# Performance work log

Hardware: AMD Instinct MI355X
Metric: run time of the kernel (lower is better)

## Reference

```python
import jax, jax.numpy as jnp
import numpy as np

DIM_MODEL = 1024
NUM_HEADS = 16
HEAD_DIM = DIM_MODEL // NUM_HEADS
NEG = -1000000000.0


def setup_inputs() -> dict:
    key = jax.random.key(0)
    ks = jax.random.split(key, 11)
    B, S, D = 2, 2048, DIM_MODEL
    s = 1.0 / np.sqrt(D)
    return {
        "q": jax.random.normal(ks[0], (B, S, D), jnp.float32),
        "k": jax.random.normal(ks[1], (B, S, D), jnp.float32),
        "v": jax.random.normal(ks[2], (B, S, D), jnp.float32),
        "Wq": jax.random.normal(ks[3], (D, D), jnp.float32) * s,
        "bq": jnp.zeros((D,), jnp.float32),
        "Wk": jax.random.normal(ks[4], (D, D), jnp.float32) * s,
        "bk": jnp.zeros((D,), jnp.float32),
        "Wv": jax.random.normal(ks[5], (D, D), jnp.float32) * s,
        "bv": jnp.zeros((D,), jnp.float32),
        "Wo": jax.random.normal(ks[6], (D, D), jnp.float32) * s,
        "bo": jnp.zeros((D,), jnp.float32),
    }


def reference(q, k, v, Wq, bq, Wk, bk, Wv, bv, Wo, bo):
    B, S, D = q.shape
    H, hd = NUM_HEADS, HEAD_DIM

    def proj(x, W, b):
        # torch Linear: x @ W.T + b, then split heads -> [B, H, S, hd]
        y = jnp.einsum("bsd,ed->bse", x, W) + b
        return y.reshape(B, S, H, hd).transpose(0, 2, 1, 3)

    qh = proj(q, Wq, bq)
    kh = proj(k, Wk, bk)
    vh = proj(v, Wv, bv)

    scores = jnp.einsum("bhqd,bhkd->bhqk", qh, kh) / np.sqrt(hd)
    # torch.triu(ones(S,S), diagonal=0): upper triangle INCLUDING diagonal is masked
    mask = jnp.triu(jnp.ones((S, S), bool))
    scores = jnp.where(mask, NEG, scores)
    # softmax over dim=-2 (query axis), as in the original module
    attn = jax.nn.softmax(scores, axis=-2)
    ctx = jnp.einsum("bhqk,bhkd->bhqd", attn, vh)  # [B,H,S,hd]
    ctx = ctx.transpose(0, 2, 1, 3).reshape(B, S, D)
    return jnp.einsum("bsd,ed->bse", ctx, Wo) + bo
```

## Files before the change

kernel.cpp:

```cpp
#include <hip/hip_runtime.h>

typedef __bf16 bf16;
typedef __attribute__((ext_vector_type(8))) __bf16 bf16x8;
typedef __attribute__((ext_vector_type(2))) __bf16 bf16x2;
typedef __attribute__((ext_vector_type(4))) float f32x4;

#define AS1 __attribute__((address_space(1)))
#define AS3 __attribute__((address_space(3)))

#define BB 2
#define SS 2048
#define DD 1024
#define HH 16
#define HD 64
#define BH (BB*HH)

#define QSCALE 0.1803368801111244f

static __device__ __forceinline__ f32x4 mfma16(bf16x8 a, bf16x8 b, f32x4 c) {
  return __builtin_amdgcn_mfma_f32_16x16x32_bf16(a, b, c, 0, 0, 0);
}
static __device__ __forceinline__ float fexp2(float x) {
  return __builtin_amdgcn_exp2f(x);
}

static __device__ __forceinline__ void swz512(int bid, int& bh, int& pr) {
  int c = bid & 7, j = bid >> 3;
  bh = c + 8 * (j & 3);
  pr = j >> 2;
}
static __device__ __forceinline__ void swz1024(int bid, int& bh, int& strip0, int& qh) {
  int c = bid & 7, j = bid >> 3;
  bh = c + 8 * (j & 3);
  int rem = j >> 2;
  strip0 = rem & 15;
  qh = rem >> 4;
}

__global__ __launch_bounds__(256) void cvt_w(const float* __restrict__ s0, const float* __restrict__ s1,
                                             const float* __restrict__ s2, const float* __restrict__ s3,
                                             bf16* __restrict__ o0, bf16* __restrict__ o1,
                                             bf16* __restrict__ o2, bf16* __restrict__ o3) {
  const int z = blockIdx.y;
  const float* s = (z == 0) ? s0 : (z == 1) ? s1 : (z == 2) ? s2 : s3;
  bf16* o = (z == 0) ? o0 : (z == 1) ? o1 : (z == 2) ? o2 : o3;
  int i = blockIdx.x * 256 + threadIdx.x;
  const float4* sp = (const float4*)s;
  float4 a = sp[2 * i], b = sp[2 * i + 1];
  bf16x8 v;
  v[0] = (bf16)a.x; v[1] = (bf16)a.y; v[2] = (bf16)a.z; v[3] = (bf16)a.w;
  v[4] = (bf16)b.x; v[5] = (bf16)b.y; v[6] = (bf16)b.z; v[7] = (bf16)b.w;
  ((bf16x8*)o)[i] = v;
}

__global__ __launch_bounds__(256) void cvt_x(const float* __restrict__ s0, const float* __restrict__ s1,
                                             const float* __restrict__ s2,
                                             bf16* __restrict__ o0, bf16* __restrict__ o1,
                                             bf16* __restrict__ o2) {
  const int z = blockIdx.y;
  const float* s = (z == 0) ? s0 : (z == 1) ? s1 : s2;
  bf16* o = (z == 0) ? o0 : (z == 1) ? o1 : o2;
  int i = blockIdx.x * 256 + threadIdx.x;
  const float4* sp = (const float4*)s;
  float4 a = sp[2 * i], b = sp[2 * i + 1];
  bf16x8 v;
  v[0] = (bf16)a.x; v[1] = (bf16)a.y; v[2] = (bf16)a.z; v[3] = (bf16)a.w;
  v[4] = (bf16)b.x; v[5] = (bf16)b.y; v[6] = (bf16)b.z; v[7] = (bf16)b.w;
  ((bf16x8*)o)[i] = v;
}

__device__ __forceinline__ void gemm_core(const bf16* __restrict__ A,
                                          const bf16* __restrict__ Bm, int K,
                                          int m0, int n0, int w, int l,
                                          bf16* sA, bf16* sB, f32x4 (&acc)[4][4]) {
  const int l15 = l & 15, lg = l >> 4;
  const int wr = (w >> 1) * 64, wc = (w & 1) * 64;
  for (int kt = 0; kt < K; kt += 32) {
#pragma unroll
    for (int i = 0; i < 2; ++i) {
      int t = i * 256 + w * 64 + l;
      const bf16* ga = A + (size_t)(m0 + (t >> 2)) * K + kt + (t & 3) * 8;
      const bf16* gb = Bm + (size_t)(n0 + (t >> 2)) * K + kt + (t & 3) * 8;
      __builtin_amdgcn_global_load_lds((const AS1 void*)ga,
                                       (AS3 void*)(sA + (i * 256 + w * 64) * 8), 16, 0, 0);
      __builtin_amdgcn_global_load_lds((const AS1 void*)gb,
                                       (AS3 void*)(sB + (i * 256 + w * 64) * 8), 16, 0, 0);
    }
    __syncthreads();
    bf16x8 af[4], bfr[4];
#pragma unroll
    for (int m = 0; m < 4; ++m)
      af[m] = *(const bf16x8*)(sA + (wr + m * 16 + l15) * 32 + lg * 8);
#pragma unroll
    for (int n = 0; n < 4; ++n)
      bfr[n] = *(const bf16x8*)(sB + (wc + n * 16 + l15) * 32 + lg * 8);
#pragma unroll
    for (int m = 0; m < 4; ++m)
#pragma unroll
      for (int n = 0; n < 4; ++n)
        acc[m][n] = mfma16(af[m], bfr[n], acc[m][n]);
    __syncthreads();
  }
}

__global__ __launch_bounds__(256) void proj_gemm(
    const bf16* __restrict__ Xq, const bf16* __restrict__ Xk, const bf16* __restrict__ Xv,
    const bf16* __restrict__ Wq, const bf16* __restrict__ Wk, const bf16* __restrict__ Wv,
    const float* __restrict__ bq, const float* __restrict__ bk, const float* __restrict__ bv,
    bf16* __restrict__ Oq, bf16* __restrict__ Ok, bf16* __restrict__ Ovt) {
  __shared__ __align__(16) bf16 sA[128 * 32];
  __shared__ __align__(16) bf16 sB[128 * 32];
  const int z = blockIdx.z;
  const bf16* A = (z == 0) ? Xq : ((z == 1) ? Xk : Xv);
  const bf16* W = (z == 0) ? Wq : ((z == 1) ? Wk : Wv);
  const float* bias = (z == 0) ? bq : ((z == 1) ? bk : bv);
  const int tid = threadIdx.x, l = tid & 63, w = tid >> 6;
  const int m0 = blockIdx.y * 128, n0 = blockIdx.x * 128;
  f32x4 acc[4][4] = {};
  gemm_core(A, W, DD, m0, n0, w, l, sA, sB, acc);
  const int l15 = l & 15, lg = l >> 4;
  const int wr = (w >> 1) * 64, wc = (w & 1) * 64;
#pragma unroll
  for (int n = 0; n < 4; ++n) {
    int col = n0 + wc + n * 16 + l15;
    float bb = bias[col];
    int h = col >> 6, d = col & 63;
#pragma unroll
    for (int m = 0; m < 4; ++m) {
#pragma unroll
      for (int r = 0; r < 4; ++r) {
        int row = m0 + wr + m * 16 + lg * 4 + r;
        int b = row >> 11, s = row & (SS - 1);
        float vv = acc[m][n][r] + bb;
        if (z == 0) vv *= QSCALE;
        if (z != 2)
          ((z == 0) ? Oq : Ok)[(((size_t)(b * HH + h)) * SS + s) * HD + d] = (bf16)vv;
        else
          Ovt[(((size_t)(b * HH + h)) * HD + d) * SS + s] = (bf16)vv;
      }
    }
  }
}

__global__ __launch_bounds__(256) void out_gemm(const bf16* __restrict__ A,
                                                const bf16* __restrict__ W,
                                                const float* __restrict__ bias,
                                                float* __restrict__ out) {
  __shared__ __align__(16) bf16 sA[128 * 32];
  __shared__ __align__(16) bf16 sB[128 * 32];
  const int tid = threadIdx.x, l = tid & 63, w = tid >> 6;
  const int m0 = blockIdx.y * 128, n0 = blockIdx.x * 128;
  f32x4 acc[4][4] = {};
  gemm_core(A, W, DD, m0, n0, w, l, sA, sB, acc);
  const int l15 = l & 15, lg = l >> 4;
  const int wr = (w >> 1) * 64, wc = (w & 1) * 64;
#pragma unroll
  for (int n = 0; n < 4; ++n) {
    int col = n0 + wc + n * 16 + l15;
    float bb = bias[col];
#pragma unroll
    for (int m = 0; m < 4; ++m)
#pragma unroll
      for (int r = 0; r < 4; ++r) {
        int row = m0 + wr + m * 16 + lg * 4 + r;
        out[(size_t)row * DD + col] = acc[m][n][r] + bb;
      }
  }
}

__global__ __launch_bounds__(256) void colz(const bf16* __restrict__ Qb,
                                            const bf16* __restrict__ Kb,
                                            float* __restrict__ zPart) {
  __shared__ float zred[4][64];
  int bh, pair, qh;
  swz1024(blockIdx.x, bh, pair, qh);
  const int tid = threadIdx.x, l = tid & 63, w = tid >> 6;
  const int l15 = l & 15, lg = l >> 4;
  const bf16* Q = Qb + (size_t)bh * SS * HD;
  const bf16* Kh = Kb + (size_t)bh * SS * HD;

  for (int half = 0; half < 2; ++half) {
    const int s = half ? (31 - pair) : pair;
    const int c0 = s * 64;
    bf16x8 kf[4][2];
#pragma unroll
    for (int kt = 0; kt < 4; ++kt) {
      kf[kt][0] = *(const bf16x8*)&Kh[(c0 + kt * 16 + l15) * HD + lg * 8];
      kf[kt][1] = *(const bf16x8*)&Kh[(c0 + kt * 16 + l15) * HD + 32 + lg * 8];
    }
    float z[4] = {};
    const int qstart = c0 + qh * 64 + w * 16;
    bf16x8 qa0, qa1, qn0, qn1;
    if (qstart < SS) {
      qa0 = *(const bf16x8*)&Q[(qstart + l15) * HD + lg * 8];
      qa1 = *(const bf16x8*)&Q[(qstart + l15) * HD + 32 + lg * 8];
    }
    for (int qb = qstart; qb < SS; qb += 128) {
      const int qnext = qb + 128;
      if (qnext < SS) {
        qn0 = *(const bf16x8*)&Q[(qnext + l15) * HD + lg * 8];
        qn1 = *(const bf16x8*)&Q[(qnext + l15) * HD + 32 + lg * 8];
      }
      f32x4 d[4] = {};
#pragma unroll
      for (int kt = 0; kt < 4; ++kt) {
        d[kt] = mfma16(qa0, kf[kt][0], d[kt]);
        d[kt] = mfma16(qa1, kf[kt][1], d[kt]);
      }
#pragma unroll
      for (int kt = 0; kt < 4; ++kt) {
        const int kcol = c0 + kt * 16 + l15;
#pragma unroll
        for (int r = 0; r < 4; ++r) {
          int qq = qb + lg * 4 + r;
          z[kt] += (qq > kcol) ? fexp2(d[kt][r]) : 0.f;
        }
      }
      qa0 = qn0; qa1 = qn1;
    }
#pragma unroll
    for (int kt = 0; kt < 4; ++kt) {
      z[kt] += __shfl_xor(z[kt], 16);
      z[kt] += __shfl_xor(z[kt], 32);
    }
    if (l < 16) {
#pragma unroll
      for (int kt = 0; kt < 4; ++kt) zred[w][kt * 16 + l15] = z[kt];
    }
    __syncthreads();
    if (tid < 64) {
      float zs = zred[0][tid] + zred[1][tid] + zred[2][tid] + zred[3][tid];
      zPart[((size_t)qh * BH + bh) * SS + c0 + tid] = zs;
    }
    __syncthreads();
  }
}

__global__ __launch_bounds__(256, 2) void attn_ctx(const bf16* __restrict__ Qb,
                                                   const bf16* __restrict__ Kb,
                                                   const bf16* __restrict__ Vt,
                                                   const float* __restrict__ zPart,
                                                   bf16* __restrict__ ctx) {
  __shared__ __align__(16) float red[3][64 * 68];
  int bh, pr;
  swz512(blockIdx.x, bh, pr);
  const int tid = threadIdx.x, l = tid & 63, w = tid >> 6;
  const int l15 = l & 15, lg = l >> 4;
  const bf16* Q = Qb + (size_t)bh * SS * HD;
  const bf16* Kh = Kb + (size_t)bh * SS * HD;
  const bf16* V = Vt + (size_t)bh * HD * SS;
  const float* zp0 = zPart + (size_t)bh * SS;
  const float* zp1 = zPart + ((size_t)BH + bh) * SS;
  const int b = bh >> 4, h = bh & 15;

  float vlast[4];
#pragma unroll
  for (int dt = 0; dt < 4; ++dt)
    vlast[dt] = (float)V[(size_t)(dt * 16 + l15) * SS + (SS - 1)] * (1.0f / (float)SS);

  for (int half = 0; half < 2; ++half) {
    const int t = half ? (31 - pr) : pr;
    const int q0 = t * 64;

    bf16x8 qa[4][2];
#pragma unroll
    for (int qt = 0; qt < 4; ++qt)
#pragma unroll
      for (int kk = 0; kk < 2; ++kk)
        qa[qt][kk] = *(const bf16x8*)&Q[(q0 + qt * 16 + l15) * HD + kk * 32 + lg * 8];

    f32x4 acc[4][4] = {};
    const int kend = q0 + 64;
    for (int k0 = w * 32; k0 < kend; k0 += 128) {
      bf16x8 ka0 = *(const bf16x8*)&Kh[(k0 + l15) * HD + lg * 8];
      bf16x8 ka1 = *(const bf16x8*)&Kh[(k0 + l15) * HD + 32 + lg * 8];
      bf16x8 kb0 = *(const bf16x8*)&Kh[(k0 + 16 + l15) * HD + lg * 8];
      bf16x8 kb1 = *(const bf16x8*)&Kh[(k0 + 16 + l15) * HD + 32 + lg * 8];
      union { unsigned int u[4]; bf16x8 v; } vf[4];
#pragma unroll
      for (int dt = 0; dt < 4; ++dt) {
        const bf16* vrow = &V[(size_t)(dt * 16 + l15) * SS];
        uint2 lo = *(const uint2*)&vrow[k0 + 4 * lg];
        uint2 hi = *(const uint2*)&vrow[k0 + 16 + 4 * lg];
        vf[dt].u[0] = lo.x; vf[dt].u[1] = lo.y; vf[dt].u[2] = hi.x; vf[dt].u[3] = hi.y;
      }
      f32x4 za0 = *(const f32x4*)&zp0[k0 + lg * 4];
      f32x4 zb0 = *(const f32x4*)&zp1[k0 + lg * 4];
      f32x4 za1 = *(const f32x4*)&zp0[k0 + 16 + lg * 4];
      f32x4 zb1 = *(const f32x4*)&zp1[k0 + 16 + lg * 4];
      f32x4 rz0, rz1;
#pragma unroll
      for (int r = 0; r < 4; ++r) {
        float s0 = za0[r] + zb0[r], s1 = za1[r] + zb1[r];
        rz0[r] = (s0 > 0.f) ? 1.0f / s0 : 0.f;
        rz1[r] = (s1 > 0.f) ? 1.0f / s1 : 0.f;
      }
      f32x4 s[4][2];
#pragma unroll
      for (int qt = 0; qt < 4; ++qt) {
        f32x4 z0 = {}, z1 = {};
        z0 = mfma16(ka0, qa[qt][0], z0);
        z0 = mfma16(ka1, qa[qt][1], z0);
        z1 = mfma16(kb0, qa[qt][0], z1);
        z1 = mfma16(kb1, qa[qt][1], z1);
        s[qt][0] = z0; s[qt][1] = z1;
      }
      const int kb0i = k0 + lg * 4, kb1i = k0 + 16 + lg * 4;
#pragma unroll
      for (int qt = 0; qt < 4; ++qt) {
        const int qq = q0 + qt * 16 + l15;
        union { unsigned int u[4]; bf16x8 v; } pa;
#pragma unroll
        for (int hw = 0; hw < 2; ++hw) {
          bf16x2 t0, t1;
#pragma unroll
          for (int r = 0; r < 2; ++r) {
            int rr = hw * 2 + r;
            float p0 = fexp2(s[qt][0][rr]) * ((kb0i + rr < qq) ? rz0[rr] : 0.f);
            float p1 = fexp2(s[qt][1][rr]) * ((kb1i + rr < qq) ? rz1[rr] : 0.f);
            t0[r] = (bf16)p0;
            t1[r] = (bf16)p1;
          }
          pa.u[hw] = __builtin_bit_cast(unsigned int, t0);
          pa.u[hw + 2] = __builtin_bit_cast(unsigned int, t1);
        }
#pragma unroll
        for (int dt = 0; dt < 4; ++dt)
          acc[qt][dt] = mfma16(pa.v, vf[dt].v, acc[qt][dt]);
      }
    }

    if (w) {
      float* buf = red[w - 1];
#pragma unroll
      for (int qt = 0; qt < 4; ++qt)
#pragma unroll
        for (int dt = 0; dt < 4; ++dt)
          *(f32x4*)&buf[(dt * 16 + l15) * 68 + qt * 16 + lg * 4] = acc[qt][dt];
    }
    __syncthreads();
    if (w == 0) {
#pragma unroll
      for (int qt = 0; qt < 4; ++qt) {
#pragma unroll
        for (int dt = 0; dt < 4; ++dt) {
          f32x4 a = acc[qt][dt];
#pragma unroll
          for (int j = 0; j < 3; ++j)
            a += *(const f32x4*)&red[j][(dt * 16 + l15) * 68 + qt * 16 + lg * 4];
#pragma unroll
          for (int r = 0; r < 4; ++r) {
            int q = q0 + qt * 16 + lg * 4 + r;
            ctx[((size_t)(b * SS + q)) * DD + h * HD + dt * 16 + l15] =
                (bf16)(a[r] + vlast[dt]);
          }
        }
      }
    }
    __syncthreads();
  }
}

extern "C" void kernel_launch(void* const* d_in, const int* in_sizes, int n_in,
                              void* d_out, int out_size, void* d_ws, size_t ws_size,
                              hipStream_t stream) {
  const float* q  = (const float*)d_in[0];
  const float* k  = (const float*)d_in[1];
  const float* v  = (const float*)d_in[2];
  const float* Wq = (const float*)d_in[3];
  const float* bq = (const float*)d_in[4];
  const float* Wk = (const float*)d_in[5];
  const float* bk = (const float*)d_in[6];
  const float* Wv = (const float*)d_in[7];
  const float* bv = (const float*)d_in[8];
  const float* Wo = (const float*)d_in[9];
  const float* bo = (const float*)d_in[10];

  char* ws = (char*)d_ws;
  const size_t SZP = (size_t)4096 * 1024 * 2;
  const size_t SZW = (size_t)1024 * 1024 * 2;
  bf16* Qb   = (bf16*)(ws + 0 * SZP);
  bf16* Kb   = (bf16*)(ws + 1 * SZP);
  bf16* Vt   = (bf16*)(ws + 2 * SZP);
  bf16* ctxb = (bf16*)(ws + 3 * SZP);
  bf16* qb16 = (bf16*)(ws + 4 * SZP);
  bf16* kb16 = (bf16*)(ws + 5 * SZP);
  bf16* vb16 = (bf16*)(ws + 6 * SZP);
  bf16* Wqb  = (bf16*)(ws + 7 * SZP + 0 * SZW);
  bf16* Wkb  = (bf16*)(ws + 7 * SZP + 1 * SZW);
  bf16* Wvb  = (bf16*)(ws + 7 * SZP + 2 * SZW);
  bf16* Wob  = (bf16*)(ws + 7 * SZP + 3 * SZW);
  float* zPart = (float*)(ws + 7 * SZP + 4 * SZW);

  cvt_w<<<dim3(512, 4), 256, 0, stream>>>(Wq, Wk, Wv, Wo, Wqb, Wkb, Wvb, Wob);
  cvt_x<<<dim3(2048, 3), 256, 0, stream>>>(q, k, v, qb16, kb16, vb16);

  proj_gemm<<<dim3(1024 / 128, 4096 / 128, 3), 256, 0, stream>>>(
      qb16, kb16, vb16, Wqb, Wkb, Wvb, bq, bk, bv, Qb, Kb, Vt);

  colz<<<1024, 256, 0, stream>>>(Qb, Kb, zPart);
  attn_ctx<<<512, 256, 0, stream>>>(Qb, Kb, Vt, zPart, ctxb);

  out_gemm<<<dim3(1024 / 128, 4096 / 128), 256, 0, stream>>>(ctxb, Wob, bo, (float*)d_out);
}
```

Before: 170.3 us.

## Halve attention query tile, precompute column reciprocals, specialize diagonal chunk

The attention-context kernel now processes 32-query tiles instead of 64, launching 1024 blocks with a higher occupancy hint and a smaller LDS reduction buffer. A new small kernel finalizes the column-sum reciprocals once, so attention blocks no longer recompute them. The key loop is split so that only the diagonal chunk applies the causal mask, handled by one wave. Smaller tiles reload K/V more often per query and add an extra launch, in exchange for more parallelism and less masking and divide work in the inner loop.

```diff
diff --git a/kernel.cpp b/kernel.cpp
--- a/kernel.cpp
+++ b/kernel.cpp
@@ -24,17 +24,17 @@
   return __builtin_amdgcn_exp2f(x);
 }
 
-static __device__ __forceinline__ void swz512(int bid, int& bh, int& pr) {
-  int c = bid & 7, j = bid >> 3;
-  bh = c + 8 * (j & 3);
-  pr = j >> 2;
-}
 static __device__ __forceinline__ void swz1024(int bid, int& bh, int& strip0, int& qh) {
   int c = bid & 7, j = bid >> 3;
   bh = c + 8 * (j & 3);
   int rem = j >> 2;
   strip0 = rem & 15;
   qh = rem >> 4;
+}
+static __device__ __forceinline__ void swzA(int bid, int& bh, int& pr) {
+  int c = bid & 7, j = bid >> 3;
+  bh = c + 8 * (j & 3);
+  pr = j >> 2;
 }
 
 __global__ __launch_bounds__(256) void cvt_w(const float* __restrict__ s0, const float* __restrict__ s1,
@@ -236,21 +236,89 @@
   }
 }
 
-__global__ __launch_bounds__(256, 2) void attn_ctx(const bf16* __restrict__ Qb,
+__global__ __launch_bounds__(256) void rzfin(const float* __restrict__ zPart,
+                                             float* __restrict__ cRZ) {
+  int i = blockIdx.x * 256 + threadIdx.x;
+  f32x4 a = ((const f32x4*)zPart)[i];
+  f32x4 b = ((const f32x4*)(zPart + (size_t)BH * SS))[i];
+  f32x4 r;
+#pragma unroll
+  for (int j = 0; j < 4; ++j) {
+    float s = a[j] + b[j];
+    r[j] = (s > 0.f) ? 1.0f / s : 0.f;
+  }
+  ((f32x4*)cRZ)[i] = r;
+}
+
+template <bool DIAG>
+static __device__ __forceinline__ void attn_chunk(
+    const bf16* __restrict__ Kh, const bf16* __restrict__ V,
+    const float* __restrict__ rzp, int k0, int q0,
+    const bf16x8 (&qa)[2][2], f32x4 (&acc)[2][4], int l15, int lg) {
+  bf16x8 ka0 = *(const bf16x8*)&Kh[(k0 + l15) * HD + lg * 8];
+  bf16x8 ka1 = *(const bf16x8*)&Kh[(k0 + l15) * HD + 32 + lg * 8];
+  bf16x8 kb0 = *(const bf16x8*)&Kh[(k0 + 16 + l15) * HD + lg * 8];
+  bf16x8 kb1 = *(const bf16x8*)&Kh[(k0 + 16 + l15) * HD + 32 + lg * 8];
+  union U { unsigned int u[4]; bf16x8 v; };
+  U vf[4];
+#pragma unroll
+  for (int dt = 0; dt < 4; ++dt) {
+    const bf16* vrow = &V[(size_t)(dt * 16 + l15) * SS];
+    uint2 lo = *(const uint2*)&vrow[k0 + 4 * lg];
+    uint2 hi = *(const uint2*)&vrow[k0 + 16 + 4 * lg];
+    vf[dt].u[0] = lo.x; vf[dt].u[1] = lo.y; vf[dt].u[2] = hi.x; vf[dt].u[3] = hi.y;
+  }
+  f32x4 rz0 = *(const f32x4*)&rzp[k0 + lg * 4];
+  f32x4 rz1 = *(const f32x4*)&rzp[k0 + 16 + lg * 4];
+  f32x4 s[2][2];
+#pragma unroll
+  for (int qt = 0; qt < 2; ++qt) {
+    f32x4 z0 = {}, z1 = {};
+    z0 = mfma16(ka0, qa[qt][0], z0);
+    z0 = mfma16(ka1, qa[qt][1], z0);
+    z1 = mfma16(kb0, qa[qt][0], z1);
+    z1 = mfma16(kb1, qa[qt][1], z1);
+    s[qt][0] = z0; s[qt][1] = z1;
+  }
+  const int kb0i = k0 + lg * 4, kb1i = k0 + 16 + lg * 4;
+#pragma unroll
+  for (int qt = 0; qt < 2; ++qt) {
+    const int qq = q0 + qt * 16 + l15;
+    U pa;
+#pragma unroll
+    for (int hw = 0; hw < 2; ++hw) {
+      bf16x2 t0, t1;
+#pragma unroll
+      for (int r = 0; r < 2; ++r) {
+        int rr = hw * 2 + r;
+        float m0 = DIAG ? ((kb0i + rr < qq) ? rz0[rr] : 0.f) : rz0[rr];
+        float m1 = DIAG ? ((kb1i + rr < qq) ? rz1[rr] : 0.f) : rz1[rr];
+        t0[r] = (bf16)(fexp2(s[qt][0][rr]) * m0);
+        t1[r] = (bf16)(fexp2(s[qt][1][rr]) * m1);
+      }
+      pa.u[hw] = __builtin_bit_cast(unsigned int, t0);
+      pa.u[hw + 2] = __builtin_bit_cast(unsigned int, t1);
+    }
+#pragma unroll
+    for (int dt = 0; dt < 4; ++dt)
+      acc[qt][dt] = mfma16(pa.v, vf[dt].v, acc[qt][dt]);
+  }
+}
+
+__global__ __launch_bounds__(256, 4) void attn_ctx(const bf16* __restrict__ Qb,
                                                    const bf16* __restrict__ Kb,
                                                    const bf16* __restrict__ Vt,
-                                                   const float* __restrict__ zPart,
+                                                   const float* __restrict__ cRZ,
                                                    bf16* __restrict__ ctx) {
-  __shared__ __align__(16) float red[3][64 * 68];
+  __shared__ __align__(16) float red[3][64 * 36];
   int bh, pr;
-  swz512(blockIdx.x, bh, pr);
+  swzA(blockIdx.x, bh, pr);
   const int tid = threadIdx.x, l = tid & 63, w = tid >> 6;
   const int l15 = l & 15, lg = l >> 4;
   const bf16* Q = Qb + (size_t)bh * SS * HD;
   const bf16* Kh = Kb + (size_t)bh * SS * HD;
   const bf16* V = Vt + (size_t)bh * HD * SS;
-  const float* zp0 = zPart + (size_t)bh * SS;
-  const float* zp1 = zPart + ((size_t)BH + bh) * SS;
+  const float* rzp = cRZ + (size_t)bh * SS;
   const int b = bh >> 4, h = bh & 15;
 
   float vlast[4];
@@ -259,95 +327,40 @@
     vlast[dt] = (float)V[(size_t)(dt * 16 + l15) * SS + (SS - 1)] * (1.0f / (float)SS);
 
   for (int half = 0; half < 2; ++half) {
-    const int t = half ? (31 - pr) : pr;
-    const int q0 = t * 64;
-
-    bf16x8 qa[4][2];
-#pragma unroll
-    for (int qt = 0; qt < 4; ++qt)
+    const int t = half ? (63 - pr) : pr;
+    const int q0 = t * 32;
+
+    bf16x8 qa[2][2];
+#pragma unroll
+    for (int qt = 0; qt < 2; ++qt)
 #pragma unroll
       for (int kk = 0; kk < 2; ++kk)
         qa[qt][kk] = *(const bf16x8*)&Q[(q0 + qt * 16 + l15) * HD + kk * 32 + lg * 8];
 
-    f32x4 acc[4][4] = {};
-    const int kend = q0 + 64;
-    for (int k0 = w * 32; k0 < kend; k0 += 128) {
-      bf16x8 ka0 = *(const bf16x8*)&Kh[(k0 + l15) * HD + lg * 8];
-      bf16x8 ka1 = *(const bf16x8*)&Kh[(k0 + l15) * HD + 32 + lg * 8];
-      bf16x8 kb0 = *(const bf16x8*)&Kh[(k0 + 16 + l15) * HD + lg * 8];
-      bf16x8 kb1 = *(const bf16x8*)&Kh[(k0 + 16 + l15) * HD + 32 + lg * 8];
-      union { unsigned int u[4]; bf16x8 v; } vf[4];
-#pragma unroll
-      for (int dt = 0; dt < 4; ++dt) {
-        const bf16* vrow = &V[(size_t)(dt * 16 + l15) * SS];
-        uint2 lo = *(const uint2*)&vrow[k0 + 4 * lg];
-        uint2 hi = *(const uint2*)&vrow[k0 + 16 + 4 * lg];
-        vf[dt].u[0] = lo.x; vf[dt].u[1] = lo.y; vf[dt].u[2] = hi.x; vf[dt].u[3] = hi.y;
-      }
-      f32x4 za0 = *(const f32x4*)&zp0[k0 + lg * 4];
-      f32x4 zb0 = *(const f32x4*)&zp1[k0 + lg * 4];
-      f32x4 za1 = *(const f32x4*)&zp0[k0 + 16 + lg * 4];
-      f32x4 zb1 = *(const f32x4*)&zp1[k0 + 16 + lg * 4];
-      f32x4 rz0, rz1;
-#pragma unroll
-      for (int r = 0; r < 4; ++r) {
-        float s0 = za0[r] + zb0[r], s1 = za1[r] + zb1[r];
-        rz0[r] = (s0 > 0.f) ? 1.0f / s0 : 0.f;
-        rz1[r] = (s1 > 0.f) ? 1.0f / s1 : 0.f;
-      }
-      f32x4 s[4][2];
-#pragma unroll
-      for (int qt = 0; qt < 4; ++qt) {
-        f32x4 z0 = {}, z1 = {};
-        z0 = mfma16(ka0, qa[qt][0], z0);
-        z0 = mfma16(ka1, qa[qt][1], z0);
-        z1 = mfma16(kb0, qa[qt][0], z1);
-        z1 = mfma16(kb1, qa[qt][1], z1);
-        s[qt][0] = z0; s[qt][1] = z1;
-      }
-      const int kb0i = k0 + lg * 4, kb1i = k0 + 16 + lg * 4;
-#pragma unroll
-      for (int qt = 0; qt < 4; ++qt) {
-        const int qq = q0 + qt * 16 + l15;
-        union { unsigned int u[4]; bf16x8 v; } pa;
-#pragma unroll
-        for (int hw = 0; hw < 2; ++hw) {
-          bf16x2 t0, t1;
-#pragma unroll
-          for (int r = 0; r < 2; ++r) {
-            int rr = hw * 2 + r;
-            float p0 = fexp2(s[qt][0][rr]) * ((kb0i + rr < qq) ? rz0[rr] : 0.f);
-            float p1 = fexp2(s[qt][1][rr]) * ((kb1i + rr < qq) ? rz1[rr] : 0.f);
-            t0[r] = (bf16)p0;
-            t1[r] = (bf16)p1;
-          }
-          pa.u[hw] = __builtin_bit_cast(unsigned int, t0);
-          pa.u[hw + 2] = __builtin_bit_cast(unsigned int, t1);
-        }
-#pragma unroll
-        for (int dt = 0; dt < 4; ++dt)
-          acc[qt][dt] = mfma16(pa.v, vf[dt].v, acc[qt][dt]);
-      }
-    }
+    f32x4 acc[2][4] = {};
+    for (int k0 = w * 32; k0 < q0; k0 += 128)
+      attn_chunk<false>(Kh, V, rzp, k0, q0, qa, acc, l15, lg);
+    if (w == (t & 3))
+      attn_chunk<true>(Kh, V, rzp, q0, q0, qa, acc, l15, lg);
 
     if (w) {
       float* buf = red[w - 1];
 #pragma unroll
-      for (int qt = 0; qt < 4; ++qt)
+      for (int qt = 0; qt < 2; ++qt)
 #pragma unroll
         for (int dt = 0; dt < 4; ++dt)
-          *(f32x4*)&buf[(dt * 16 + l15) * 68 + qt * 16 + lg * 4] = acc[qt][dt];
+          *(f32x4*)&buf[(dt * 16 + l15) * 36 + qt * 16 + lg * 4] = acc[qt][dt];
     }
     __syncthreads();
     if (w == 0) {
 #pragma unroll
-      for (int qt = 0; qt < 4; ++qt) {
+      for (int qt = 0; qt < 2; ++qt) {
 #pragma unroll
         for (int dt = 0; dt < 4; ++dt) {
           f32x4 a = acc[qt][dt];
 #pragma unroll
           for (int j = 0; j < 3; ++j)
-            a += *(const f32x4*)&red[j][(dt * 16 + l15) * 68 + qt * 16 + lg * 4];
+            a += *(const f32x4*)&red[j][(dt * 16 + l15) * 36 + qt * 16 + lg * 4];
 #pragma unroll
           for (int r = 0; r < 4; ++r) {
             int q = q0 + qt * 16 + lg * 4 + r;
@@ -391,6 +404,7 @@
   bf16* Wvb  = (bf16*)(ws + 7 * SZP + 2 * SZW);
   bf16* Wob  = (bf16*)(ws + 7 * SZP + 3 * SZW);
   float* zPart = (float*)(ws + 7 * SZP + 4 * SZW);
+  float* cRZ   = zPart + (size_t)2 * BH * SS;
 
   cvt_w<<<dim3(512, 4), 256, 0, stream>>>(Wq, Wk, Wv, Wo, Wqb, Wkb, Wvb, Wob);
   cvt_x<<<dim3(2048, 3), 256, 0, stream>>>(q, k, v, qb16, kb16, vb16);
@@ -399,7 +413,8 @@
       qb16, kb16, vb16, Wqb, Wkb, Wvb, bq, bk, bv, Qb, Kb, Vt);
 
   colz<<<1024, 256, 0, stream>>>(Qb, Kb, zPart);
-  attn_ctx<<<512, 256, 0, stream>>>(Qb, Kb, Vt, zPart, ctxb);
+  rzfin<<<(BH * SS / 4) / 256, 256, 0, stream>>>(zPart, cRZ);
+  attn_ctx<<<1024, 256, 0, stream>>>(Qb, Kb, Vt, cRZ, ctxb);
 
   out_gemm<<<dim3(1024 / 128, 4096 / 128), 256, 0, stream>>>(ctxb, Wob, bo, (float*)d_out);
 }
```

Result: slower. 214.5 us (+26.0%).

## Fold column-softmax reciprocal into V and double-buffer K/V loads in attn_ctx

Applied to the files above, without the earlier changes.

Adds two small kernels. One finalizes the per-key reciprocal column sums, and the other scales the transposed V in place by those reciprocals while also capturing the last-row V values. This removes the zPart loads, reciprocal math and per-element multiply from the attention inner loop. The inner loop now uses software-pipelined A/B register buffers for the K/V loads, and the causal mask is applied only to the diagonal 64-key tile, which is split between two waves. The cost is two extra launches, an extra pass over V, more register pressure, and the diagonal work now falling on only two of the four waves.

```diff
diff --git a/kernel.cpp b/kernel.cpp
--- a/kernel.cpp
+++ b/kernel.cpp
@@ -236,10 +236,107 @@
   }
 }
 
+__global__ __launch_bounds__(256) void rzfin(const float* __restrict__ zPart,
+                                             float* __restrict__ cRZ) {
+  int i = blockIdx.x * 256 + threadIdx.x;
+  f32x4 a = ((const f32x4*)zPart)[i];
+  f32x4 b = ((const f32x4*)(zPart + (size_t)BH * SS))[i];
+  f32x4 r;
+#pragma unroll
+  for (int j = 0; j < 4; ++j) {
+    float s = a[j] + b[j];
+    r[j] = (s > 0.f) ? 1.0f / s : 0.f;
+  }
+  ((f32x4*)cRZ)[i] = r;
+}
+
+__global__ __launch_bounds__(256) void vscale(bf16* __restrict__ Vt,
+                                              const float* __restrict__ cRZ,
+                                              float* __restrict__ vlastB) {
+  int i = blockIdx.x * 256 + threadIdx.x;
+  int sc = i & (SS / 8 - 1);
+  int rest = i >> 8;
+  int s0 = sc * 8;
+  bf16* p = Vt + (size_t)rest * SS + s0;
+  const float* rz = cRZ + (size_t)(rest >> 6) * SS + s0;
+  bf16x8 v = *(const bf16x8*)p;
+  if (s0 + 8 == SS) vlastB[rest] = (float)v[7] * (1.0f / (float)SS);
+  f32x4 r0 = *(const f32x4*)rz, r1 = *(const f32x4*)(rz + 4);
+  bf16x8 o;
+#pragma unroll
+  for (int j = 0; j < 4; ++j) o[j] = (bf16)((float)v[j] * r0[j]);
+#pragma unroll
+  for (int j = 0; j < 4; ++j) o[4 + j] = (bf16)((float)v[4 + j] * r1[j]);
+  *(bf16x8*)p = o;
+}
+
+struct KV {
+  bf16x8 k[4];
+  unsigned int v[4][4];
+};
+
+static __device__ __forceinline__ void kv_load(KV& b, const bf16* __restrict__ Kh,
+                                               const bf16* __restrict__ V, int k0,
+                                               int l15, int lg) {
+  b.k[0] = *(const bf16x8*)&Kh[(k0 + l15) * HD + lg * 8];
+  b.k[1] = *(const bf16x8*)&Kh[(k0 + l15) * HD + 32 + lg * 8];
+  b.k[2] = *(const bf16x8*)&Kh[(k0 + 16 + l15) * HD + lg * 8];
+  b.k[3] = *(const bf16x8*)&Kh[(k0 + 16 + l15) * HD + 32 + lg * 8];
+#pragma unroll
+  for (int dt = 0; dt < 4; ++dt) {
+    const bf16* vrow = &V[(size_t)(dt * 16 + l15) * SS];
+    uint2 lo = *(const uint2*)&vrow[k0 + 4 * lg];
+    uint2 hi = *(const uint2*)&vrow[k0 + 16 + 4 * lg];
+    b.v[dt][0] = lo.x; b.v[dt][1] = lo.y; b.v[dt][2] = hi.x; b.v[dt][3] = hi.y;
+  }
+}
+
+template <bool DIAG>
+static __device__ __forceinline__ void kv_compute(const KV& b, int k0, int q0,
+                                                  const bf16x8 (&qa)[4][2],
+                                                  f32x4 (&acc)[4][4], int l15, int lg) {
+  const int kb0i = k0 + lg * 4, kb1i = k0 + 16 + lg * 4;
+#pragma unroll
+  for (int qt = 0; qt < 4; ++qt) {
+    f32x4 s0 = {}, s1 = {};
+    s0 = mfma16(b.k[0], qa[qt][0], s0);
+    s0 = mfma16(b.k[1], qa[qt][1], s0);
+    s1 = mfma16(b.k[2], qa[qt][0], s1);
+    s1 = mfma16(b.k[3], qa[qt][1], s1);
+    const int qq = q0 + qt * 16 + l15;
+    union { unsigned int u[4]; bf16x8 v; } pa;
+#pragma unroll
+    for (int hw = 0; hw < 2; ++hw) {
+      bf16x2 t0, t1;
+#pragma unroll
+      for (int r = 0; r < 2; ++r) {
+        int rr = hw * 2 + r;
+        float p0 = fexp2(s0[rr]);
+        float p1 = fexp2(s1[rr]);
+        if (DIAG) {
+          p0 = (kb0i + rr < qq) ? p0 : 0.f;
+          p1 = (kb1i + rr < qq) ? p1 : 0.f;
+        }
+        t0[r] = (bf16)p0;
+        t1[r] = (bf16)p1;
+      }
+      pa.u[hw] = __builtin_bit_cast(unsigned int, t0);
+      pa.u[hw + 2] = __builtin_bit_cast(unsigned int, t1);
+    }
+#pragma unroll
+    for (int dt = 0; dt < 4; ++dt) {
+      union { unsigned int u[4]; bf16x8 v; } vf;
+      vf.u[0] = b.v[dt][0]; vf.u[1] = b.v[dt][1];
+      vf.u[2] = b.v[dt][2]; vf.u[3] = b.v[dt][3];
+      acc[qt][dt] = mfma16(pa.v, vf.v, acc[qt][dt]);
+    }
+  }
+}
+
 __global__ __launch_bounds__(256, 2) void attn_ctx(const bf16* __restrict__ Qb,
                                                    const bf16* __restrict__ Kb,
                                                    const bf16* __restrict__ Vt,
-                                                   const float* __restrict__ zPart,
+                                                   const float* __restrict__ vlastB,
                                                    bf16* __restrict__ ctx) {
   __shared__ __align__(16) float red[3][64 * 68];
   int bh, pr;
@@ -249,14 +346,11 @@
   const bf16* Q = Qb + (size_t)bh * SS * HD;
   const bf16* Kh = Kb + (size_t)bh * SS * HD;
   const bf16* V = Vt + (size_t)bh * HD * SS;
-  const float* zp0 = zPart + (size_t)bh * SS;
-  const float* zp1 = zPart + ((size_t)BH + bh) * SS;
   const int b = bh >> 4, h = bh & 15;
 
   float vlast[4];
 #pragma unroll
-  for (int dt = 0; dt < 4; ++dt)
-    vlast[dt] = (float)V[(size_t)(dt * 16 + l15) * SS + (SS - 1)] * (1.0f / (float)SS);
+  for (int dt = 0; dt < 4; ++dt) vlast[dt] = vlastB[bh * 64 + dt * 16 + l15];
 
   for (int half = 0; half < 2; ++half) {
     const int t = half ? (31 - pr) : pr;
@@ -270,63 +364,28 @@
         qa[qt][kk] = *(const bf16x8*)&Q[(q0 + qt * 16 + l15) * HD + kk * 32 + lg * 8];
 
     f32x4 acc[4][4] = {};
-    const int kend = q0 + 64;
-    for (int k0 = w * 32; k0 < kend; k0 += 128) {
-      bf16x8 ka0 = *(const bf16x8*)&Kh[(k0 + l15) * HD + lg * 8];
-      bf16x8 ka1 = *(const bf16x8*)&Kh[(k0 + l15) * HD + 32 + lg * 8];
-      bf16x8 kb0 = *(const bf16x8*)&Kh[(k0 + 16 + l15) * HD + lg * 8];
-      bf16x8 kb1 = *(const bf16x8*)&Kh[(k0 + 16 + l15) * HD + 32 + lg * 8];
-      union { unsigned int u[4]; bf16x8 v; } vf[4];
-#pragma unroll
-      for (int dt = 0; dt < 4; ++dt) {
-        const bf16* vrow = &V[(size_t)(dt * 16 + l15) * SS];
-        uint2 lo = *(const uint2*)&vrow[k0 + 4 * lg];
-        uint2 hi = *(const uint2*)&vrow[k0 + 16 + 4 * lg];
-        vf[dt].u[0] = lo.x; vf[dt].u[1] = lo.y; vf[dt].u[2] = hi.x; vf[dt].u[3] = hi.y;
-      }
-      f32x4 za0 = *(const f32x4*)&zp0[k0 + lg * 4];
-      f32x4 zb0 = *(const f32x4*)&zp1[k0 + lg * 4];
-      f32x4 za1 = *(const f32x4*)&zp0[k0 + 16 + lg * 4];
-      f32x4 zb1 = *(const f32x4*)&zp1[k0 + 16 + lg * 4];
-      f32x4 rz0, rz1;
-#pragma unroll
-      for (int r = 0; r < 4; ++r) {
-        float s0 = za0[r] + zb0[r], s1 = za1[r] + zb1[r];
-        rz0[r] = (s0 > 0.f) ? 1.0f / s0 : 0.f;
-        rz1[r] = (s1 > 0.f) ? 1.0f / s1 : 0.f;
-      }
-      f32x4 s[4][2];
-#pragma unroll
-      for (int qt = 0; qt < 4; ++qt) {
-        f32x4 z0 = {}, z1 = {};
-        z0 = mfma16(ka0, qa[qt][0], z0);
-        z0 = mfma16(ka1, qa[qt][1], z0);
-        z1 = mfma16(kb0, qa[qt][0], z1);
-        z1 = mfma16(kb1, qa[qt][1], z1);
-        s[qt][0] = z0; s[qt][1] = z1;
-      }
-      const int kb0i = k0 + lg * 4, kb1i = k0 + 16 + lg * 4;
-#pragma unroll
-      for (int qt = 0; qt < 4; ++qt) {
-        const int qq = q0 + qt * 16 + l15;
-        union { unsigned int u[4]; bf16x8 v; } pa;
-#pragma unroll
-        for (int hw = 0; hw < 2; ++hw) {
-          bf16x2 t0, t1;
-#pragma unroll
-          for (int r = 0; r < 2; ++r) {
-            int rr = hw * 2 + r;
-            float p0 = fexp2(s[qt][0][rr]) * ((kb0i + rr < qq) ? rz0[rr] : 0.f);
-            float p1 = fexp2(s[qt][1][rr]) * ((kb1i + rr < qq) ? rz1[rr] : 0.f);
-            t0[r] = (bf16)p0;
-            t1[r] = (bf16)p1;
-          }
-          pa.u[hw] = __builtin_bit_cast(unsigned int, t0);
-          pa.u[hw + 2] = __builtin_bit_cast(unsigned int, t1);
-        }
-#pragma unroll
-        for (int dt = 0; dt < 4; ++dt)
-          acc[qt][dt] = mfma16(pa.v, vf[dt].v, acc[qt][dt]);
+    KV A, B;
+    int k0 = w * 32;
+    if (k0 < q0) {
+      kv_load(A, Kh, V, k0, l15, lg);
+      for (;;) {
+        int kn = k0 + 128;
+        if (kn >= q0) { kv_compute<false>(A, k0, q0, qa, acc, l15, lg); break; }
+        kv_load(B, Kh, V, kn, l15, lg);
+        kv_compute<false>(A, k0, q0, qa, acc, l15, lg);
+        k0 = kn; kn += 128;
+        if (kn >= q0) { kv_compute<false>(B, k0, q0, qa, acc, l15, lg); break; }
+        kv_load(A, Kh, V, kn, l15, lg);
+        kv_compute<false>(B, k0, q0, qa, acc, l15, lg);
+        k0 = kn;
+      }
+    }
+    {
+      const int cw = (2 * t) & 3;
+      int dk = (w == cw) ? q0 : ((w == ((cw + 1) & 3)) ? q0 + 32 : -1);
+      if (dk >= 0) {
+        kv_load(A, Kh, V, dk, l15, lg);
+        kv_compute<true>(A, dk, q0, qa, acc, l15, lg);
       }
     }
 
@@ -391,6 +450,8 @@
   bf16* Wvb  = (bf16*)(ws + 7 * SZP + 2 * SZW);
   bf16* Wob  = (bf16*)(ws + 7 * SZP + 3 * SZW);
   float* zPart = (float*)(ws + 7 * SZP + 4 * SZW);
+  float* cRZ   = zPart + (size_t)2 * BH * SS;
+  float* vlastB = cRZ + (size_t)BH * SS;
 
   cvt_w<<<dim3(512, 4), 256, 0, stream>>>(Wq, Wk, Wv, Wo, Wqb, Wkb, Wvb, Wob);
   cvt_x<<<dim3(2048, 3), 256, 0, stream>>>(q, k, v, qb16, kb16, vb16);
@@ -399,7 +460,9 @@
       qb16, kb16, vb16, Wqb, Wkb, Wvb, bq, bk, bv, Qb, Kb, Vt);
 
   colz<<<1024, 256, 0, stream>>>(Qb, Kb, zPart);
-  attn_ctx<<<512, 256, 0, stream>>>(Qb, Kb, Vt, zPart, ctxb);
+  rzfin<<<(BH * SS / 4) / 256, 256, 0, stream>>>(zPart, cRZ);
+  vscale<<<(BH * HD * SS / 8) / 256, 256, 0, stream>>>(Vt, cRZ, vlastB);
+  attn_ctx<<<512, 256, 0, stream>>>(Qb, Kb, Vt, vlastB, ctxb);
 
   out_gemm<<<dim3(1024 / 128, 4096 / 128), 256, 0, stream>>>(ctxb, Wob, bo, (float*)d_out);
 }
```

New measurement: 174.5 us. 1.02x slower.
